# Kernel tuning notes

Measured on AMD Instinct MI355X. Metric: run time of the kernel, lower is better.

## Reference

```python
import jax, jax.numpy as jnp
from jax import lax
import numpy as np

D_MODEL = 768
D_STATE = 16
D_CONV = 4
EXPAND = 2
D_INNER = EXPAND * D_MODEL
BATCH = 2
SEQ = 512


def setup_inputs() -> dict:
    key = jax.random.key(0)
    ks = jax.random.split(key, 8)
    s = 0.02
    return {
        "x": jax.random.normal(ks[0], (BATCH, SEQ, D_MODEL), jnp.float32),
        "W_in": jax.random.normal(ks[1], (2 * D_INNER, D_MODEL), jnp.float32) * s,
        "conv_w": jax.random.normal(ks[2], (D_INNER, 1, D_CONV), jnp.float32) * s,
        "conv_b": jnp.zeros((D_INNER,), jnp.float32),
        "W_x": jax.random.normal(ks[3], (D_INNER + 2 * D_STATE, D_INNER), jnp.float32) * s,
        "W_dt": jax.random.normal(ks[4], (D_INNER, D_INNER), jnp.float32) * s,
        "b_dt": jnp.zeros((D_INNER,), jnp.float32),
        "A_log": jnp.log(jax.random.uniform(ks[5], (D_INNER, D_STATE), jnp.float32, 1e-4, 1.0)),
        "Dp": jnp.ones((D_INNER,), jnp.float32),
        "W_out": jax.random.normal(ks[6], (D_MODEL, D_INNER), jnp.float32) * s,
    }


def parallel_scan_log(log_coeffs, log_values):
    """Faithful port of ParallelScan.parallel_scan_log (Blelchh-style up/down sweep
    in log space). Indices are static, so the Python loop over O(log L) levels is
    trace-time only."""
    B, L, D = log_coeffs.shape
    if L <= 4:
        run = log_values[:, 0]
        outs = [run]
        for i in range(1, L):
            run = jnp.logaddexp(run, log_coeffs[:, i] + log_values[:, i])
            outs.append(run)
        return jnp.stack(outs, axis=1)
    levels = int(np.ceil(np.log2(L)))
    coeffs, values = log_coeffs, log_values
    # up-sweep
    for level in range(levels):
        step = 2 ** (level + 1)
        if step - 1 >= L:
            break
        right = np.arange(step - 1, L, step)
        left = right - 2 ** level
        m = (left >= 0) & (right < L)
        left, right = left[m], right[m]
        if left.size == 0:
            continue
        new_c = coeffs[:, left] + coeffs[:, right]
        new_v = jnp.logaddexp(values[:, left], coeffs[:, right] + values[:, right])
        coeffs = coeffs.at[:, right].set(new_c)
        values = values.at[:, right].set(new_v)
    # down-sweep
    for level in range(levels - 1, -1, -1):
        step = 2 ** (level + 1)
        if step - 1 >= L:
            continue
        right = np.arange(step - 1, L, step)
        left = right - 2 ** level
        m = (left >= 0) & (right < L)
        left, right = left[m], right[m]
        if left.size == 0:
            continue
        tmp = values[:, right]
        new_r = jnp.logaddexp(values[:, left], coeffs[:, right] + values[:, right])
        values = values.at[:, right].set(new_r)
        values = values.at[:, left].set(tmp)
    return values


def reference(x, W_in, conv_w, conv_b, W_x, W_dt, b_dt, A_log, Dp, W_out):
    Bsz, L, _ = x.shape
    xz = x @ W_in.T                                 # [B, L, 2*d_inner]
    x_inner, z = jnp.split(xz, 2, axis=-1)
    # depthwise causal conv1d (pad left d_conv-1, truncate to L == torch slice)
    xc = jnp.transpose(x_inner, (0, 2, 1))          # [B, d_inner, L]
    xc = lax.conv_general_dilated(
        xc, conv_w, (1,), [(D_CONV - 1, 0)],
        dimension_numbers=("NCH", "OIH", "NCH"),
        feature_group_count=D_INNER)
    xc = xc + conv_b[None, :, None]
    x_conv = jax.nn.silu(jnp.transpose(xc, (0, 2, 1)))  # [B, L, d_inner]
    x_dbl = x_conv @ W_x.T                              # [B, L, d_inner + 2*d_state]
    delta, Bmat, Cmat = jnp.split(x_dbl, [D_INNER, D_INNER + D_STATE], axis=-1)
    delta = jax.nn.softplus(delta @ W_dt.T + b_dt)      # [B, L, d_inner]
    # selective scan
    A = -jnp.exp(A_log)                                 # [d_inner, d_state]
    deltaA = jnp.exp(jnp.einsum("bld,dn->bldn", delta, A))
    deltaB_u = jnp.einsum("bld,bln,bld->bldn", delta, Bmat, x_conv)
    log_coeffs = jnp.log(deltaA + 1e-12).reshape(Bsz, L, -1)
    log_values = jnp.log(jnp.abs(deltaB_u) + 1e-12).reshape(Bsz, L, -1)
    scanned = jnp.exp(parallel_scan_log(log_coeffs, log_values))
    scanned = scanned.reshape(Bsz, L, D_INNER, D_STATE)
    y = jnp.einsum("bldn,bln->bld", scanned, Cmat) + x_conv * Dp
    y = y * jax.nn.silu(z)
    return y @ W_out.T
```

## Files before the change

kernel.cpp:

```cpp
#include <hip/hip_runtime.h>
#include <math.h>

#define D_MODEL 768
#define D_STATE 16
#define D_CONV  4
#define D_INNER 1536
#define BATCH   2
#define SEQ     512
#define M_ROWS  (BATCH * SEQ)
#define N_XZ    (2 * D_INNER)
#define N_XDBL  (D_INNER + 2 * D_STATE)

typedef _Float16 half8 __attribute__((ext_vector_type(8)));
typedef float  f32x4  __attribute__((ext_vector_type(4)));
typedef unsigned short ushort_t;
typedef ushort_t ushort8_t __attribute__((ext_vector_type(8)));

__device__ __forceinline__ ushort_t f2h(float f) {
    _Float16 h = (_Float16)f;
    return *(ushort_t*)&h;
}
__device__ __forceinline__ float h2f(ushort_t u) {
    return (float)(*(const _Float16*)&u);
}
__device__ __forceinline__ void pack8(const float* s, ushort_t* d) {
    ushort8_t o;
#pragma unroll
    for (int j = 0; j < 8; ++j) o[j] = f2h(s[j]);
    *(ushort8_t*)d = o;
}
__device__ __forceinline__ void gld16(const ushort_t* g, void* l) {
    __builtin_amdgcn_global_load_lds((const __attribute__((address_space(1))) void*)g,
                                     (__attribute__((address_space(3))) void*)l, 16, 0, 0);
}

#define SX   (M_ROWS * D_MODEL)
#define SW1  (N_XZ * D_MODEL)
#define SW2  (N_XDBL * D_INNER)
#define SWDT (D_INNER * D_INNER)
#define SWO  (D_MODEL * D_INNER)
#define SPACK (SX + SW1 + SW2 + SWDT + SWO)
__global__ __launch_bounds__(256) void pack_kernel(
    const float* __restrict__ x, const float* __restrict__ win,
    const float* __restrict__ wx, const float* __restrict__ wdt,
    const float* __restrict__ wo,
    ushort_t* __restrict__ xs, ushort_t* __restrict__ w1, ushort_t* __restrict__ w2,
    ushort_t* __restrict__ wdt16, ushort_t* __restrict__ wo16)
{
    long i = ((long)blockIdx.x * 256 + threadIdx.x) * 8;
    if (i >= SPACK) return;
    const float* src; ushort_t* dst; long base;
    if (i < SX)                         { src = x;   dst = xs;    base = i; }
    else if (i < SX + SW1)              { src = win; dst = w1;    base = i - SX; }
    else if (i < SX + SW1 + SW2)        { src = wx;  dst = w2;    base = i - SX - SW1; }
    else if (i < SX + SW1 + SW2 + SWDT) { src = wdt; dst = wdt16; base = i - SX - SW1 - SW2; }
    else                                { src = wo;  dst = wo16;  base = i - SX - SW1 - SW2 - SWDT; }
    float v[8];
    *(float4*)(v)     = *(const float4*)(src + base);
    *(float4*)(v + 4) = *(const float4*)(src + base + 4);
    pack8(v, dst + base);
}

template<int HALF_OUT>
__global__ __launch_bounds__(512, 6) void gemm_lds(
    const ushort_t* __restrict__ A, int lda,
    const ushort_t* __restrict__ B, int ldb,
    void* __restrict__ Cbase, long pstride, int ldc,
    int N, int kc)
{
    __shared__ ushort_t smA[3][4096];
    __shared__ ushort_t smB[3][4096];

    const int tid  = threadIdx.x;
    const int w    = tid >> 6;
    const int lane = tid & 63;
    const int lr   = lane & 15;
    const int lq   = lane >> 4;

    const int Gx = gridDim.x, Gy = gridDim.y;
    const int T = Gx * Gy * gridDim.z;
    const int f = blockIdx.x + Gx * (blockIdx.y + Gy * blockIdx.z);
    const int g = (T & 7) ? f : ((f & 7) * (T >> 3) + (f >> 3));
    const int bx = g % Gx;
    const int by = (g / Gx) % Gy;
    const int z  = g / (Gx * Gy);
    ushort_t* __restrict__ Ch = (ushort_t*)Cbase + (long)z * pstride;
    float*    __restrict__ Cf = (float*)Cbase + (long)z * pstride;

    const int bm = by * 128;
    const int bn = bx * 128;
    const int k0base = z * kc;

    auto stage = [&](int buf, int k0) {
        {
            const int rA = bm + w * 16 + lr;
            gld16(A + (long)rA * lda + k0 + lq * 8, &smA[buf][w * 512]);
        }
        {
            int rB = bn + w * 16 + lr; if (rB >= N) rB = N - 1;
            gld16(B + (long)rB * ldb + k0 + lq * 8, &smB[buf][w * 512]);
        }
    };

    f32x4 acc[4][2] = {};
    const int wm = (w & 1) * 64;
    const int wn = (w >> 1) * 32;

    const int nIter = kc >> 5;
    stage(0, k0base);
    int cur = 0;
    for (int it = 0; it < nIter; ++it) {
        const int nxt = (cur == 2) ? 0 : cur + 1;
        if (it + 1 < nIter) {
            stage(nxt, k0base + (it + 1) * 32);
            asm volatile("s_waitcnt vmcnt(2)" ::: "memory");
        } else {
            asm volatile("s_waitcnt vmcnt(0)" ::: "memory");
        }
        __builtin_amdgcn_s_barrier();
        asm volatile("" ::: "memory");

        half8 ah[4], bh[2];
#pragma unroll
        for (int mt = 0; mt < 4; ++mt)
            ah[mt] = *(const half8*)&smA[cur][(((w & 1) * 4 + mt) * 512) + lq * 128 + lr * 8];
#pragma unroll
        for (int nt = 0; nt < 2; ++nt)
            bh[nt] = *(const half8*)&smB[cur][(((w >> 1) * 2 + nt) * 512) + lq * 128 + lr * 8];
#pragma unroll
        for (int mt = 0; mt < 4; ++mt)
#pragma unroll
            for (int nt = 0; nt < 2; ++nt)
                acc[mt][nt] = __builtin_amdgcn_mfma_f32_16x16x32_f16(ah[mt], bh[nt], acc[mt][nt], 0, 0, 0);
        cur = nxt;
    }

#pragma unroll
    for (int mt = 0; mt < 4; ++mt)
#pragma unroll
        for (int nt = 0; nt < 2; ++nt)
#pragma unroll
            for (int r = 0; r < 4; ++r) {
                int row = bm + wm + mt * 16 + lq * 4 + r;
                int col = bn + wn + nt * 16 + lr;
                if (col >= N) continue;
                if (HALF_OUT) Ch[(long)row * ldc + col] = f2h(acc[mt][nt][r]);
                else          Cf[(long)row * ldc + col] = acc[mt][nt][r];
            }
}

__global__ __launch_bounds__(256) void conv_silu_kernel(
    const ushort_t* __restrict__ P, long ps,
    const float* __restrict__ conv_w, const float* __restrict__ conv_b,
    float* __restrict__ xconvT, float* __restrict__ zsiluT,
    ushort_t* __restrict__ xc)
{
    __shared__ float Tx[64][17];
    __shared__ float Tz[64][17];
    const int rb = blockIdx.x;
    const int db = blockIdx.y;
    const int dl = threadIdx.x & 63;
    const int d  = db * 64 + dl;
    const int rr = threadIdx.x >> 6;
    const float w0 = conv_w[d * 4 + 0], w1 = conv_w[d * 4 + 1];
    const float w2 = conv_w[d * 4 + 2], w3 = conv_w[d * 4 + 3];
    const float bb = conv_b[d];
    auto mrg = [&](long o) {
        return h2f(P[o]) + h2f(P[o + ps]) + h2f(P[o + 2 * ps]) + h2f(P[o + 3 * ps]);
    };
#pragma unroll
    for (int q = 0; q < 4; ++q) {
        const int r = rb * 16 + q * 4 + rr;
        const int l = r & (SEQ - 1);
        float acc = bb;
        if (l >= 3) acc = fmaf(w0, mrg((long)(r - 3) * N_XZ + d), acc);
        if (l >= 2) acc = fmaf(w1, mrg((long)(r - 2) * N_XZ + d), acc);
        if (l >= 1) acc = fmaf(w2, mrg((long)(r - 1) * N_XZ + d), acc);
        acc = fmaf(w3, mrg((long)r * N_XZ + d), acc);
        float s = acc / (1.f + expf(-acc));
        xc[(long)r * D_INNER + d] = f2h(s);
        float zv = mrg((long)r * N_XZ + D_INNER + d);
        Tx[dl][q * 4 + rr] = s;
        Tz[dl][q * 4 + rr] = zv / (1.f + expf(-zv));
    }
    __syncthreads();
    const int rp = threadIdx.x & 15;
    const int dp = threadIdx.x >> 4;
#pragma unroll
    for (int p = 0; p < 4; ++p) {
        int dd = p * 16 + dp;
        long o = (long)(db * 64 + dd) * M_ROWS + rb * 16 + rp;
        xconvT[o] = Tx[dd][rp];
        zsiluT[o] = Tz[dd][rp];
    }
}

__global__ __launch_bounds__(256) void ep_xdbl_kernel(
    const float* __restrict__ P, long ps,
    ushort_t* __restrict__ xd, float* __restrict__ BCT)
{
    long i = ((long)blockIdx.x * 256 + threadIdx.x) * 8;
    if (i >= (long)M_ROWS * N_XDBL) return;
    int row = (int)(i / N_XDBL);
    int col = (int)(i - (long)row * N_XDBL);
    float f[8];
#pragma unroll
    for (int j = 0; j < 8; ++j)
        f[j] = P[i + j] + P[i + j + ps] + P[i + j + 2 * ps] + P[i + j + 3 * ps];
    pack8(f, xd + i);
    if (col >= D_INNER) {
#pragma unroll
        for (int j = 0; j < 8; ++j)
            BCT[(long)(col + j - D_INNER) * M_ROWS + row] = f[j];
    }
}

__global__ __launch_bounds__(256) void ep_merge_kernel(
    const ushort_t* __restrict__ P, long ps, float* __restrict__ out)
{
    long i = ((long)blockIdx.x * 256 + threadIdx.x) * 8;
    if (i >= (long)M_ROWS * D_MODEL) return;
    float o[8] = {};
#pragma unroll
    for (int z = 0; z < 16; ++z) {
        ushort8_t v = *(const ushort8_t*)(P + i + z * ps);
#pragma unroll
        for (int j = 0; j < 8; ++j) o[j] += h2f(v[j]);
    }
    *(float4*)(out + i)     = *(float4*)(o);
    *(float4*)(out + i + 4) = *(float4*)(o + 4);
}

__global__ __launch_bounds__(256) void scan_kernel(
    const ushort_t* __restrict__ P, long ps,
    const float* __restrict__ b_dt,
    const float* __restrict__ xconvT,
    const float* __restrict__ zsiluT,
    const float* __restrict__ BCT,
    const float* __restrict__ A_log,
    const float* __restrict__ Dp,
    ushort_t* __restrict__ uT)
{
    __shared__ float dlT[512];
    __shared__ float xrT[512];
    __shared__ float red[3 * 512];

    const int bid = blockIdx.x;
    const int b   = bid / D_INNER;
    const int d   = bid % D_INNER;
    const int tid = threadIdx.x;
    const int w   = tid >> 6;
    const int t   = tid & 63;
    const long od = (long)d * M_ROWS + b * SEQ;

    const float bdt = b_dt[d];
#pragma unroll
    for (int q = 0; q < 2; ++q) {
        const int l = tid + q * 256;
        float v = bdt;
#pragma unroll
        for (int z = 0; z < 8; ++z) v += h2f(P[od + l + z * ps]);
        float sp = fmaxf(v, 0.f) + log1pf(expf(-fabsf(v)));
        const int li = (l & 7) * 64 + (l >> 3);
        dlT[li] = sp;
        xrT[li] = xconvT[od + l];
    }
    __syncthreads();

    float dl[8], xr[8], dx[8], yac[8];
#pragma unroll
    for (int j = 0; j < 8; ++j) {
        dl[j] = dlT[j * 64 + t];
        xr[j] = xrT[j * 64 + t];
        dx[j] = dl[j] * xr[j];
        yac[j] = 0.f;
    }
    const int l0 = 8 * t;

#pragma unroll
    for (int nn = 0; nn < 4; ++nn) {
        const int n = w * 4 + nn;
        const float Adn = -expf(A_log[d * D_STATE + n]);
        const float4* Bp = (const float4*)(BCT + (long)n * M_ROWS + b * SEQ + l0);
        float4 b0 = Bp[0], b1 = Bp[1];
        float Bv[8] = {b0.x, b0.y, b0.z, b0.w, b1.x, b1.y, b1.z, b1.w};
        float c[8], v[8];
#pragma unroll
        for (int j = 0; j < 8; ++j) {
            c[j] = __expf(dl[j] * Adn);
            v[j] = fabsf(dx[j] * Bv[j]);
        }
        float c01 = c[1] * c[0], v01 = fmaf(c[1], v[0], v[1]);
        float c23 = c[3] * c[2], v23 = fmaf(c[3], v[2], v[3]);
        float c45 = c[5] * c[4], v45 = fmaf(c[5], v[4], v[5]);
        float c67 = c[7] * c[6], v67 = fmaf(c[7], v[6], v[7]);
        float c03 = c23 * c01,  v03 = fmaf(c23, v01, v23);
        float c47 = c67 * c45,  v47 = fmaf(c67, v45, v67);
        float cA  = c47 * c03,  vA  = fmaf(c47, v03, v47);
#pragma unroll
        for (int h = 1; h <= 32; h <<= 1) {
            float cl = __shfl_up(cA, (unsigned)h);
            float vl = __shfl_up(vA, (unsigned)h);
            if (t >= h) { vA = fmaf(cA, vl, vA); cA = cA * cl; }
        }
        float s = __shfl_up(vA, 1u);
        if (t == 0) s = 0.f;
        const float4* Cp = (const float4*)(BCT + (long)(16 + n) * M_ROWS + b * SEQ + l0);
        float4 c0 = Cp[0], c1 = Cp[1];
        float Cv[8] = {c0.x, c0.y, c0.z, c0.w, c1.x, c1.y, c1.z, c1.w};
#pragma unroll
        for (int j = 0; j < 8; ++j) {
            s = fmaf(c[j], s, v[j]);
            yac[j] = fmaf(s, Cv[j], yac[j]);
        }
    }

    if (w) {
#pragma unroll
        for (int j = 0; j < 8; ++j) red[(w - 1) * 512 + j * 64 + t] = yac[j];
    }
    __syncthreads();
    if (w == 0) {
        const float Dpd = Dp[d];
        ushort8_t uo;
#pragma unroll
        for (int j = 0; j < 8; ++j) {
            float y = yac[j] + red[j * 64 + t] + red[512 + j * 64 + t] + red[1024 + j * 64 + t];
            float uv = fmaf(xr[j], Dpd, y) * zsiluT[od + l0 + j];
            uo[j] = f2h(uv);
        }
        *(ushort8_t*)(uT + od + l0) = uo;
    }
}

__global__ __launch_bounds__(256) void transpose_split_kernel(
    const ushort_t* __restrict__ uT, ushort_t* __restrict__ u)
{
    __shared__ ushort_t T[64][65];
    const int m0 = blockIdx.x * 64;
    const int d0 = blockIdx.y * 64;
    const int c  = threadIdx.x & 63;
    const int rr = threadIdx.x >> 6;
#pragma unroll
    for (int p = 0; p < 64; p += 4)
        T[p + rr][c] = uT[(long)(d0 + p + rr) * M_ROWS + m0 + c];
    __syncthreads();
#pragma unroll
    for (int p = 0; p < 64; p += 4) {
        int rm = p + rr;
        u[(long)(m0 + rm) * D_INNER + (d0 + c)] = T[c][rm];
    }
}

extern "C" void kernel_launch(void* const* d_in, const int* in_sizes, int n_in,
                              void* d_out, int out_size, void* d_ws, size_t ws_size,
                              hipStream_t stream)
{
    (void)in_sizes; (void)n_in; (void)out_size; (void)ws_size;

    const float* x      = (const float*)d_in[0];
    const float* W_in   = (const float*)d_in[1];
    const float* conv_w = (const float*)d_in[2];
    const float* conv_b = (const float*)d_in[3];
    const float* W_x    = (const float*)d_in[4];
    const float* W_dt   = (const float*)d_in[5];
    const float* b_dt   = (const float*)d_in[6];
    const float* A_log  = (const float*)d_in[7];
    const float* Dp     = (const float*)d_in[8];
    const float* W_out  = (const float*)d_in[9];
    float* out = (float*)d_out;

    float* ws = (float*)d_ws;
    long off = 0;
    float* P      = ws + off; off += 2L * M_ROWS * N_XZ;
    float* uTbuf  = ws + off; off += (long)D_INNER * M_ROWS / 2;
    float* xconvT = ws + off; off += (long)D_INNER * M_ROWS;
    float* zsiluT = ws + off; off += (long)D_INNER * M_ROWS;
    float* xsbuf  = ws + off; off += (long)M_ROWS * D_MODEL / 2;
    float* w1buf  = ws + off; off += (long)N_XZ * D_MODEL / 2;
    float* w2buf  = ws + off; off += (long)N_XDBL * D_INNER / 2;
    float* wdtbuf = ws + off; off += (long)D_INNER * D_INNER / 2;
    float* wobuf  = ws + off; off += (long)D_MODEL * D_INNER / 2;
    float* xcbuf  = ws + off; off += (long)M_ROWS * D_INNER / 2;
    float* xdbuf  = ws + off; off += (long)M_ROWS * N_XDBL / 2;
    float* BCT    = ws + off; off += (long)2 * D_STATE * M_ROWS;

    ushort_t* xs    = (ushort_t*)xsbuf;
    ushort_t* w1    = (ushort_t*)w1buf;
    ushort_t* w2    = (ushort_t*)w2buf;
    ushort_t* wdt16 = (ushort_t*)wdtbuf;
    ushort_t* wo16  = (ushort_t*)wobuf;
    ushort_t* xc    = (ushort_t*)xcbuf;
    ushort_t* xd    = (ushort_t*)xdbuf;
    ushort_t* u_i   = (ushort_t*)xcbuf;
    ushort_t* uT    = (ushort_t*)uTbuf;
    ushort_t* P16   = (ushort_t*)P;

    const long psG1 = (long)M_ROWS * N_XZ;
    const long psG3 = (long)M_ROWS * N_XDBL;
    const long psG4 = (long)D_INNER * M_ROWS;
    const long psG6 = (long)M_ROWS * D_MODEL;

    dim3 blk(256);
    dim3 gblk(512);

    pack_kernel<<<dim3(SPACK / 2048), blk, 0, stream>>>(
        x, W_in, W_x, W_dt, W_out, xs, w1, w2, wdt16, wo16);
    gemm_lds<1><<<dim3(N_XZ / 128, M_ROWS / 128, 4), gblk, 0, stream>>>(
        xs, D_MODEL, w1, D_MODEL, P16, psG1, N_XZ, N_XZ, D_MODEL / 4);
    conv_silu_kernel<<<dim3(M_ROWS / 16, D_INNER / 64), blk, 0, stream>>>(
        P16, psG1, conv_w, conv_b, xconvT, zsiluT, xc);
    gemm_lds<0><<<dim3((N_XDBL + 127) / 128, M_ROWS / 128, 4), gblk, 0, stream>>>(
        xc, D_INNER, w2, D_INNER, P, psG3, N_XDBL, N_XDBL, D_INNER / 4);
    ep_xdbl_kernel<<<dim3((M_ROWS * N_XDBL) / 2048), blk, 0, stream>>>(
        P, psG3, xd, BCT);
    gemm_lds<1><<<dim3(M_ROWS / 128, D_INNER / 128, 8), gblk, 0, stream>>>(
        wdt16, D_INNER, xd, N_XDBL, P16, psG4, M_ROWS, M_ROWS, D_INNER / 8);
    scan_kernel<<<dim3(BATCH * D_INNER), blk, 0, stream>>>(
        P16, psG4, b_dt, xconvT, zsiluT, BCT, A_log, Dp, uT);
    transpose_split_kernel<<<dim3(M_ROWS / 64, D_INNER / 64), blk, 0, stream>>>(
        uT, u_i);
    gemm_lds<1><<<dim3(D_MODEL / 128, M_ROWS / 128, 16), gblk, 0, stream>>>(
        u_i, D_INNER, wo16, D_INNER, P16, psG6, D_MODEL, D_MODEL, D_INNER / 16);
    ep_merge_kernel<<<dim3((M_ROWS * D_MODEL) / 2048), blk, 0, stream>>>(
        P16, psG6, out);
}
```

Before: 206.8 us.

## Fuse all stages into a persistent megakernel with software grid barriers

Replaces the ten separate kernel launches with one persistent kernel of 384 blocks that runs every stage (pack, four GEMMs, conv/silu, epilogues, scan, transpose, merge) in sequence, separated by atomic-counter grid barriers. The goal is to remove launch gaps and tail effects between the many small kernels. Several per-stage parameters change along the way: the W_x GEMM split-K drops from 4 to 3, the conv and transpose tiles are retiled, and the scan handles two channels per block. The cost is that every stage runs on a fixed grid that may not match its natural parallelism, plus barrier spin overhead. The barrier depends on all 384 blocks being co-resident, and its spin loop has a timeout that could silently break synchronization.

```diff
diff --git a/kernel.cpp b/kernel.cpp
--- a/kernel.cpp
+++ b/kernel.cpp
@@ -40,52 +40,58 @@
 #define SWDT (D_INNER * D_INNER)
 #define SWO  (D_MODEL * D_INNER)
 #define SPACK (SX + SW1 + SW2 + SWDT + SWO)
-__global__ __launch_bounds__(256) void pack_kernel(
-    const float* __restrict__ x, const float* __restrict__ win,
-    const float* __restrict__ wx, const float* __restrict__ wdt,
-    const float* __restrict__ wo,
-    ushort_t* __restrict__ xs, ushort_t* __restrict__ w1, ushort_t* __restrict__ w2,
-    ushort_t* __restrict__ wdt16, ushort_t* __restrict__ wo16)
-{
-    long i = ((long)blockIdx.x * 256 + threadIdx.x) * 8;
-    if (i >= SPACK) return;
-    const float* src; ushort_t* dst; long base;
-    if (i < SX)                         { src = x;   dst = xs;    base = i; }
-    else if (i < SX + SW1)              { src = win; dst = w1;    base = i - SX; }
-    else if (i < SX + SW1 + SW2)        { src = wx;  dst = w2;    base = i - SX - SW1; }
-    else if (i < SX + SW1 + SW2 + SWDT) { src = wdt; dst = wdt16; base = i - SX - SW1 - SW2; }
-    else                                { src = wo;  dst = wo16;  base = i - SX - SW1 - SW2 - SWDT; }
-    float v[8];
-    *(float4*)(v)     = *(const float4*)(src + base);
-    *(float4*)(v + 4) = *(const float4*)(src + base + 4);
-    pack8(v, dst + base);
+
+#define PSG1 ((long)M_ROWS * N_XZ)
+#define PSG3 ((long)M_ROWS * N_XDBL)
+#define PSG4 ((long)D_INNER * M_ROWS)
+#define PSG6 ((long)M_ROWS * D_MODEL)
+
+#define NBLK 384
+
+struct Params {
+    const float *x, *W_in, *conv_w, *conv_b, *W_x, *W_dt, *b_dt, *A_log, *Dp, *W_out;
+    float* out;
+    ushort_t *xs, *w1, *w2, *wdt16, *wo16, *xc, *xd, *u_i, *uT, *P16;
+    float *Pf, *xconvT, *zsiluT, *BCT;
+    unsigned* bar;
+};
+
+__device__ __forceinline__ void grid_barrier(unsigned* bar) {
+    __syncthreads();
+    if (threadIdx.x == 0) {
+        __threadfence();
+        unsigned gen = __hip_atomic_load(bar + 1, __ATOMIC_RELAXED, __HIP_MEMORY_SCOPE_AGENT);
+        unsigned prev = __hip_atomic_fetch_add(bar, 1u, __ATOMIC_ACQ_REL, __HIP_MEMORY_SCOPE_AGENT);
+        if (prev == (unsigned)(NBLK - 1)) {
+            __hip_atomic_store(bar, 0u, __ATOMIC_RELAXED, __HIP_MEMORY_SCOPE_AGENT);
+            __hip_atomic_fetch_add(bar + 1, 1u, __ATOMIC_RELEASE, __HIP_MEMORY_SCOPE_AGENT);
+        } else {
+            long spins = 0;
+            while (__hip_atomic_load(bar + 1, __ATOMIC_RELAXED, __HIP_MEMORY_SCOPE_AGENT) == gen) {
+                __builtin_amdgcn_s_sleep(2);
+                if (++spins > (1L << 26)) break;
+            }
+        }
+        __threadfence();
+    }
+    __syncthreads();
 }
 
 template<int HALF_OUT>
-__global__ __launch_bounds__(512, 6) void gemm_lds(
+__device__ __forceinline__ void gemm_tile(
+    ushort_t* smA, ushort_t* smB,
     const ushort_t* __restrict__ A, int lda,
     const ushort_t* __restrict__ B, int ldb,
-    void* __restrict__ Cbase, long pstride, int ldc,
-    int N, int kc)
+    void* Cbase, long pstride, int ldc, int N, int kc,
+    int bx, int by, int z, int tid)
 {
-    __shared__ ushort_t smA[3][4096];
-    __shared__ ushort_t smB[3][4096];
-
-    const int tid  = threadIdx.x;
     const int w    = tid >> 6;
     const int lane = tid & 63;
     const int lr   = lane & 15;
     const int lq   = lane >> 4;
 
-    const int Gx = gridDim.x, Gy = gridDim.y;
-    const int T = Gx * Gy * gridDim.z;
-    const int f = blockIdx.x + Gx * (blockIdx.y + Gy * blockIdx.z);
-    const int g = (T & 7) ? f : ((f & 7) * (T >> 3) + (f >> 3));
-    const int bx = g % Gx;
-    const int by = (g / Gx) % Gy;
-    const int z  = g / (Gx * Gy);
-    ushort_t* __restrict__ Ch = (ushort_t*)Cbase + (long)z * pstride;
-    float*    __restrict__ Cf = (float*)Cbase + (long)z * pstride;
+    ushort_t* Ch = (ushort_t*)Cbase + (long)z * pstride;
+    float*    Cf = (float*)Cbase + (long)z * pstride;
 
     const int bm = by * 128;
     const int bn = bx * 128;
@@ -94,11 +100,11 @@
     auto stage = [&](int buf, int k0) {
         {
             const int rA = bm + w * 16 + lr;
-            gld16(A + (long)rA * lda + k0 + lq * 8, &smA[buf][w * 512]);
+            gld16(A + (long)rA * lda + k0 + lq * 8, smA + buf * 4096 + w * 512);
         }
         {
             int rB = bn + w * 16 + lr; if (rB >= N) rB = N - 1;
-            gld16(B + (long)rB * ldb + k0 + lq * 8, &smB[buf][w * 512]);
+            gld16(B + (long)rB * ldb + k0 + lq * 8, smB + buf * 4096 + w * 512);
         }
     };
 
@@ -123,10 +129,10 @@
         half8 ah[4], bh[2];
 #pragma unroll
         for (int mt = 0; mt < 4; ++mt)
-            ah[mt] = *(const half8*)&smA[cur][(((w & 1) * 4 + mt) * 512) + lq * 128 + lr * 8];
+            ah[mt] = *(const half8*)&smA[cur * 4096 + (((w & 1) * 4 + mt) * 512) + lq * 128 + lr * 8];
 #pragma unroll
         for (int nt = 0; nt < 2; ++nt)
-            bh[nt] = *(const half8*)&smB[cur][(((w >> 1) * 2 + nt) * 512) + lq * 128 + lr * 8];
+            bh[nt] = *(const half8*)&smB[cur * 4096 + (((w >> 1) * 2 + nt) * 512) + lq * 128 + lr * 8];
 #pragma unroll
         for (int mt = 0; mt < 4; ++mt)
 #pragma unroll
@@ -149,206 +155,255 @@
             }
 }
 
-__global__ __launch_bounds__(256) void conv_silu_kernel(
-    const ushort_t* __restrict__ P, long ps,
-    const float* __restrict__ conv_w, const float* __restrict__ conv_b,
-    float* __restrict__ xconvT, float* __restrict__ zsiluT,
-    ushort_t* __restrict__ xc)
+__global__ __launch_bounds__(512, 4) void mega_kernel(Params p)
 {
-    __shared__ float Tx[64][17];
-    __shared__ float Tz[64][17];
-    const int rb = blockIdx.x;
-    const int db = blockIdx.y;
-    const int dl = threadIdx.x & 63;
-    const int d  = db * 64 + dl;
-    const int rr = threadIdx.x >> 6;
-    const float w0 = conv_w[d * 4 + 0], w1 = conv_w[d * 4 + 1];
-    const float w2 = conv_w[d * 4 + 2], w3 = conv_w[d * 4 + 3];
-    const float bb = conv_b[d];
-    auto mrg = [&](long o) {
-        return h2f(P[o]) + h2f(P[o + ps]) + h2f(P[o + 2 * ps]) + h2f(P[o + 3 * ps]);
-    };
-#pragma unroll
-    for (int q = 0; q < 4; ++q) {
-        const int r = rb * 16 + q * 4 + rr;
-        const int l = r & (SEQ - 1);
-        float acc = bb;
-        if (l >= 3) acc = fmaf(w0, mrg((long)(r - 3) * N_XZ + d), acc);
-        if (l >= 2) acc = fmaf(w1, mrg((long)(r - 2) * N_XZ + d), acc);
-        if (l >= 1) acc = fmaf(w2, mrg((long)(r - 1) * N_XZ + d), acc);
-        acc = fmaf(w3, mrg((long)r * N_XZ + d), acc);
-        float s = acc / (1.f + expf(-acc));
-        xc[(long)r * D_INNER + d] = f2h(s);
-        float zv = mrg((long)r * N_XZ + D_INNER + d);
-        Tx[dl][q * 4 + rr] = s;
-        Tz[dl][q * 4 + rr] = zv / (1.f + expf(-zv));
-    }
-    __syncthreads();
-    const int rp = threadIdx.x & 15;
-    const int dp = threadIdx.x >> 4;
-#pragma unroll
-    for (int p = 0; p < 4; ++p) {
-        int dd = p * 16 + dp;
-        long o = (long)(db * 64 + dd) * M_ROWS + rb * 16 + rp;
-        xconvT[o] = Tx[dd][rp];
-        zsiluT[o] = Tz[dd][rp];
-    }
-}
-
-__global__ __launch_bounds__(256) void ep_xdbl_kernel(
-    const float* __restrict__ P, long ps,
-    ushort_t* __restrict__ xd, float* __restrict__ BCT)
-{
-    long i = ((long)blockIdx.x * 256 + threadIdx.x) * 8;
-    if (i >= (long)M_ROWS * N_XDBL) return;
-    int row = (int)(i / N_XDBL);
-    int col = (int)(i - (long)row * N_XDBL);
-    float f[8];
-#pragma unroll
-    for (int j = 0; j < 8; ++j)
-        f[j] = P[i + j] + P[i + j + ps] + P[i + j + 2 * ps] + P[i + j + 3 * ps];
-    pack8(f, xd + i);
-    if (col >= D_INNER) {
+    __shared__ __align__(16) unsigned char smem[49152];
+    ushort_t* smA = (ushort_t*)smem;
+    ushort_t* smB = (ushort_t*)(smem + 24576);
+
+    const int tid = threadIdx.x;
+    const int bid = blockIdx.x;
+    const int NB  = NBLK;
+
+    for (long v = (long)bid * 512 + tid; v < SPACK / 8; v += (long)NB * 512) {
+        long i = v * 8;
+        const float* src; ushort_t* dst; long base;
+        if (i < SX)                         { src = p.x;    dst = p.xs;    base = i; }
+        else if (i < SX + SW1)              { src = p.W_in; dst = p.w1;    base = i - SX; }
+        else if (i < SX + SW1 + SW2)        { src = p.W_x;  dst = p.w2;    base = i - SX - SW1; }
+        else if (i < SX + SW1 + SW2 + SWDT) { src = p.W_dt; dst = p.wdt16; base = i - SX - SW1 - SW2; }
+        else                                { src = p.W_out;dst = p.wo16;  base = i - SX - SW1 - SW2 - SWDT; }
+        float vv[8];
+        *(float4*)(vv)     = *(const float4*)(src + base);
+        *(float4*)(vv + 4) = *(const float4*)(src + base + 4);
+        pack8(vv, dst + base);
+    }
+    grid_barrier(p.bar);
+
+    for (int t = bid; t < 768; t += NB) {
+        gemm_tile<1>(smA, smB, p.xs, D_MODEL, p.w1, D_MODEL,
+                     p.P16, PSG1, N_XZ, N_XZ, D_MODEL / 4,
+                     t % 24, (t / 24) % 8, t / 192, tid);
+        __syncthreads();
+    }
+    grid_barrier(p.bar);
+
+    {
+        float* Tx = (float*)smem;
+        float* Tz = Tx + 64 * 33;
+        const ushort_t* P = p.P16;
+        for (int tu = bid; tu < 768; tu += NB) {
+            const int rb = tu & 31;
+            const int db = tu >> 5;
+            const int dl = tid & 63;
+            const int d  = db * 64 + dl;
+            const int rr = tid >> 6;
+            const float w0 = p.conv_w[d * 4 + 0], w1v = p.conv_w[d * 4 + 1];
+            const float w2v = p.conv_w[d * 4 + 2], w3v = p.conv_w[d * 4 + 3];
+            const float bb = p.conv_b[d];
+            auto mrg = [&](long o) {
+                return h2f(P[o]) + h2f(P[o + PSG1]) + h2f(P[o + 2 * PSG1]) + h2f(P[o + 3 * PSG1]);
+            };
+            __syncthreads();
+#pragma unroll
+            for (int q = 0; q < 4; ++q) {
+                const int r = rb * 32 + q * 8 + rr;
+                const int l = r & (SEQ - 1);
+                float acc = bb;
+                if (l >= 3) acc = fmaf(w0,  mrg((long)(r - 3) * N_XZ + d), acc);
+                if (l >= 2) acc = fmaf(w1v, mrg((long)(r - 2) * N_XZ + d), acc);
+                if (l >= 1) acc = fmaf(w2v, mrg((long)(r - 1) * N_XZ + d), acc);
+                acc = fmaf(w3v, mrg((long)r * N_XZ + d), acc);
+                float s = acc / (1.f + expf(-acc));
+                p.xc[(long)r * D_INNER + d] = f2h(s);
+                float zv = mrg((long)r * N_XZ + D_INNER + d);
+                Tx[dl * 33 + q * 8 + rr] = s;
+                Tz[dl * 33 + q * 8 + rr] = zv / (1.f + expf(-zv));
+            }
+            __syncthreads();
+            const int rp = tid & 31;
+            const int dp = (tid >> 5) & 15;
+#pragma unroll
+            for (int pp = 0; pp < 4; ++pp) {
+                int dd = pp * 16 + dp;
+                long o = (long)(db * 64 + dd) * M_ROWS + rb * 32 + rp;
+                p.xconvT[o] = Tx[dd * 33 + rp];
+                p.zsiluT[o] = Tz[dd * 33 + rp];
+            }
+        }
+    }
+    grid_barrier(p.bar);
+
+    for (int t = bid; t < 312; t += NB) {
+        gemm_tile<0>(smA, smB, p.xc, D_INNER, p.w2, D_INNER,
+                     p.Pf, PSG3, N_XDBL, N_XDBL, D_INNER / 3,
+                     t % 13, (t / 13) % 8, t / 104, tid);
+        __syncthreads();
+    }
+    grid_barrier(p.bar);
+
+    for (long v = (long)bid * 512 + tid; v < (long)M_ROWS * N_XDBL / 8; v += (long)NB * 512) {
+        long i = v * 8;
+        int row = (int)(i / N_XDBL);
+        int col = (int)(i - (long)row * N_XDBL);
+        float f[8];
 #pragma unroll
         for (int j = 0; j < 8; ++j)
-            BCT[(long)(col + j - D_INNER) * M_ROWS + row] = f[j];
-    }
-}
-
-__global__ __launch_bounds__(256) void ep_merge_kernel(
-    const ushort_t* __restrict__ P, long ps, float* __restrict__ out)
-{
-    long i = ((long)blockIdx.x * 256 + threadIdx.x) * 8;
-    if (i >= (long)M_ROWS * D_MODEL) return;
-    float o[8] = {};
-#pragma unroll
-    for (int z = 0; z < 16; ++z) {
-        ushort8_t v = *(const ushort8_t*)(P + i + z * ps);
-#pragma unroll
-        for (int j = 0; j < 8; ++j) o[j] += h2f(v[j]);
-    }
-    *(float4*)(out + i)     = *(float4*)(o);
-    *(float4*)(out + i + 4) = *(float4*)(o + 4);
-}
-
-__global__ __launch_bounds__(256) void scan_kernel(
-    const ushort_t* __restrict__ P, long ps,
-    const float* __restrict__ b_dt,
-    const float* __restrict__ xconvT,
-    const float* __restrict__ zsiluT,
-    const float* __restrict__ BCT,
-    const float* __restrict__ A_log,
-    const float* __restrict__ Dp,
-    ushort_t* __restrict__ uT)
-{
-    __shared__ float dlT[512];
-    __shared__ float xrT[512];
-    __shared__ float red[3 * 512];
-
-    const int bid = blockIdx.x;
-    const int b   = bid / D_INNER;
-    const int d   = bid % D_INNER;
-    const int tid = threadIdx.x;
-    const int w   = tid >> 6;
-    const int t   = tid & 63;
-    const long od = (long)d * M_ROWS + b * SEQ;
-
-    const float bdt = b_dt[d];
-#pragma unroll
-    for (int q = 0; q < 2; ++q) {
-        const int l = tid + q * 256;
-        float v = bdt;
-#pragma unroll
-        for (int z = 0; z < 8; ++z) v += h2f(P[od + l + z * ps]);
-        float sp = fmaxf(v, 0.f) + log1pf(expf(-fabsf(v)));
-        const int li = (l & 7) * 64 + (l >> 3);
-        dlT[li] = sp;
-        xrT[li] = xconvT[od + l];
-    }
-    __syncthreads();
-
-    float dl[8], xr[8], dx[8], yac[8];
-#pragma unroll
-    for (int j = 0; j < 8; ++j) {
-        dl[j] = dlT[j * 64 + t];
-        xr[j] = xrT[j * 64 + t];
-        dx[j] = dl[j] * xr[j];
-        yac[j] = 0.f;
-    }
-    const int l0 = 8 * t;
-
-#pragma unroll
-    for (int nn = 0; nn < 4; ++nn) {
-        const int n = w * 4 + nn;
-        const float Adn = -expf(A_log[d * D_STATE + n]);
-        const float4* Bp = (const float4*)(BCT + (long)n * M_ROWS + b * SEQ + l0);
-        float4 b0 = Bp[0], b1 = Bp[1];
-        float Bv[8] = {b0.x, b0.y, b0.z, b0.w, b1.x, b1.y, b1.z, b1.w};
-        float c[8], v[8];
-#pragma unroll
-        for (int j = 0; j < 8; ++j) {
-            c[j] = __expf(dl[j] * Adn);
-            v[j] = fabsf(dx[j] * Bv[j]);
-        }
-        float c01 = c[1] * c[0], v01 = fmaf(c[1], v[0], v[1]);
-        float c23 = c[3] * c[2], v23 = fmaf(c[3], v[2], v[3]);
-        float c45 = c[5] * c[4], v45 = fmaf(c[5], v[4], v[5]);
-        float c67 = c[7] * c[6], v67 = fmaf(c[7], v[6], v[7]);
-        float c03 = c23 * c01,  v03 = fmaf(c23, v01, v23);
-        float c47 = c67 * c45,  v47 = fmaf(c67, v45, v67);
-        float cA  = c47 * c03,  vA  = fmaf(c47, v03, v47);
-#pragma unroll
-        for (int h = 1; h <= 32; h <<= 1) {
-            float cl = __shfl_up(cA, (unsigned)h);
-            float vl = __shfl_up(vA, (unsigned)h);
-            if (t >= h) { vA = fmaf(cA, vl, vA); cA = cA * cl; }
-        }
-        float s = __shfl_up(vA, 1u);
-        if (t == 0) s = 0.f;
-        const float4* Cp = (const float4*)(BCT + (long)(16 + n) * M_ROWS + b * SEQ + l0);
-        float4 c0 = Cp[0], c1 = Cp[1];
-        float Cv[8] = {c0.x, c0.y, c0.z, c0.w, c1.x, c1.y, c1.z, c1.w};
-#pragma unroll
-        for (int j = 0; j < 8; ++j) {
-            s = fmaf(c[j], s, v[j]);
-            yac[j] = fmaf(s, Cv[j], yac[j]);
-        }
-    }
-
-    if (w) {
-#pragma unroll
-        for (int j = 0; j < 8; ++j) red[(w - 1) * 512 + j * 64 + t] = yac[j];
-    }
-    __syncthreads();
-    if (w == 0) {
-        const float Dpd = Dp[d];
-        ushort8_t uo;
-#pragma unroll
-        for (int j = 0; j < 8; ++j) {
-            float y = yac[j] + red[j * 64 + t] + red[512 + j * 64 + t] + red[1024 + j * 64 + t];
-            float uv = fmaf(xr[j], Dpd, y) * zsiluT[od + l0 + j];
-            uo[j] = f2h(uv);
-        }
-        *(ushort8_t*)(uT + od + l0) = uo;
-    }
-}
-
-__global__ __launch_bounds__(256) void transpose_split_kernel(
-    const ushort_t* __restrict__ uT, ushort_t* __restrict__ u)
-{
-    __shared__ ushort_t T[64][65];
-    const int m0 = blockIdx.x * 64;
-    const int d0 = blockIdx.y * 64;
-    const int c  = threadIdx.x & 63;
-    const int rr = threadIdx.x >> 6;
-#pragma unroll
-    for (int p = 0; p < 64; p += 4)
-        T[p + rr][c] = uT[(long)(d0 + p + rr) * M_ROWS + m0 + c];
-    __syncthreads();
-#pragma unroll
-    for (int p = 0; p < 64; p += 4) {
-        int rm = p + rr;
-        u[(long)(m0 + rm) * D_INNER + (d0 + c)] = T[c][rm];
+            f[j] = p.Pf[i + j] + p.Pf[i + j + PSG3] + p.Pf[i + j + 2 * PSG3];
+        pack8(f, p.xd + i);
+        if (col >= D_INNER) {
+#pragma unroll
+            for (int j = 0; j < 8; ++j)
+                p.BCT[(long)(col + j - D_INNER) * M_ROWS + row] = f[j];
+        }
+    }
+    grid_barrier(p.bar);
+
+    for (int t = bid; t < 768; t += NB) {
+        gemm_tile<1>(smA, smB, p.wdt16, D_INNER, p.xd, N_XDBL,
+                     p.P16, PSG4, M_ROWS, M_ROWS, D_INNER / 8,
+                     t % 8, (t / 8) % 12, t / 96, tid);
+        __syncthreads();
+    }
+    grid_barrier(p.bar);
+
+    {
+        float* S = (float*)smem;
+        const int w    = tid >> 6;
+        const int half = w >> 2;
+        const int wl   = w & 3;
+        const int t64  = tid & 63;
+        float* dlT = S + half * 2560;
+        float* xrT = dlT + 512;
+        float* red = xrT + 512;
+        for (int u = bid; u < 1536; u += NB) {
+            const int bd = 2 * u + half;
+            const int b  = bd / D_INNER;
+            const int d  = bd % D_INNER;
+            const long od = (long)d * M_ROWS + b * SEQ;
+            const float bdt = p.b_dt[d];
+            __syncthreads();
+            const int lh = tid & 255;
+#pragma unroll
+            for (int q = 0; q < 2; ++q) {
+                const int l = lh + q * 256;
+                float v = bdt;
+#pragma unroll
+                for (int z = 0; z < 8; ++z) v += h2f(p.P16[od + l + z * PSG4]);
+                float sp = fmaxf(v, 0.f) + log1pf(expf(-fabsf(v)));
+                const int li = (l & 7) * 64 + (l >> 3);
+                dlT[li] = sp;
+                xrT[li] = p.xconvT[od + l];
+            }
+            __syncthreads();
+
+            float dl[8], xr[8], dx[8], yac[8];
+#pragma unroll
+            for (int j = 0; j < 8; ++j) {
+                dl[j] = dlT[j * 64 + t64];
+                xr[j] = xrT[j * 64 + t64];
+                dx[j] = dl[j] * xr[j];
+                yac[j] = 0.f;
+            }
+            const int l0 = 8 * t64;
+#pragma unroll
+            for (int nn = 0; nn < 4; ++nn) {
+                const int n = wl * 4 + nn;
+                const float Adn = -expf(p.A_log[d * D_STATE + n]);
+                const float4* Bp = (const float4*)(p.BCT + (long)n * M_ROWS + b * SEQ + l0);
+                float4 b0 = Bp[0], b1 = Bp[1];
+                float Bv[8] = {b0.x, b0.y, b0.z, b0.w, b1.x, b1.y, b1.z, b1.w};
+                float c[8], v[8];
+#pragma unroll
+                for (int j = 0; j < 8; ++j) {
+                    c[j] = __expf(dl[j] * Adn);
+                    v[j] = fabsf(dx[j] * Bv[j]);
+                }
+                float c01 = c[1] * c[0], v01 = fmaf(c[1], v[0], v[1]);
+                float c23 = c[3] * c[2], v23 = fmaf(c[3], v[2], v[3]);
+                float c45 = c[5] * c[4], v45 = fmaf(c[5], v[4], v[5]);
+                float c67 = c[7] * c[6], v67 = fmaf(c[7], v[6], v[7]);
+                float c03 = c23 * c01,  v03 = fmaf(c23, v01, v23);
+                float c47 = c67 * c45,  v47 = fmaf(c67, v45, v67);
+                float cA  = c47 * c03,  vA  = fmaf(c47, v03, v47);
+#pragma unroll
+                for (int h = 1; h <= 32; h <<= 1) {
+                    float cl = __shfl_up(cA, (unsigned)h);
+                    float vl = __shfl_up(vA, (unsigned)h);
+                    if (t64 >= h) { vA = fmaf(cA, vl, vA); cA = cA * cl; }
+                }
+                float s = __shfl_up(vA, 1u);
+                if (t64 == 0) s = 0.f;
+                const float4* Cp = (const float4*)(p.BCT + (long)(16 + n) * M_ROWS + b * SEQ + l0);
+                float4 c0 = Cp[0], c1 = Cp[1];
+                float Cv[8] = {c0.x, c0.y, c0.z, c0.w, c1.x, c1.y, c1.z, c1.w};
+#pragma unroll
+                for (int j = 0; j < 8; ++j) {
+                    s = fmaf(c[j], s, v[j]);
+                    yac[j] = fmaf(s, Cv[j], yac[j]);
+                }
+            }
+
+            if (wl) {
+#pragma unroll
+                for (int j = 0; j < 8; ++j) red[(wl - 1) * 512 + j * 64 + t64] = yac[j];
+            }
+            __syncthreads();
+            if (wl == 0) {
+                const float Dpd = p.Dp[d];
+                ushort8_t uo;
+#pragma unroll
+                for (int j = 0; j < 8; ++j) {
+                    float y = yac[j] + red[j * 64 + t64] + red[512 + j * 64 + t64] + red[1024 + j * 64 + t64];
+                    float uv = fmaf(xr[j], Dpd, y) * p.zsiluT[od + l0 + j];
+                    uo[j] = f2h(uv);
+                }
+                *(ushort8_t*)(p.uT + od + l0) = uo;
+            }
+        }
+    }
+    grid_barrier(p.bar);
+
+    {
+        ushort_t* T = (ushort_t*)smem;
+        for (int tu = bid; tu < 384; tu += NB) {
+            const int m0 = (tu & 15) * 64;
+            const int d0 = (tu >> 4) * 64;
+            const int c  = tid & 63;
+            const int rr = tid >> 6;
+            __syncthreads();
+#pragma unroll
+            for (int pp = 0; pp < 64; pp += 8)
+                T[(pp + rr) * 65 + c] = p.uT[(long)(d0 + pp + rr) * M_ROWS + m0 + c];
+            __syncthreads();
+#pragma unroll
+            for (int pp = 0; pp < 64; pp += 8) {
+                int rm = pp + rr;
+                p.u_i[(long)(m0 + rm) * D_INNER + (d0 + c)] = T[c * 65 + rm];
+            }
+        }
+    }
+    grid_barrier(p.bar);
+
+    for (int t = bid; t < 768; t += NB) {
+        gemm_tile<1>(smA, smB, p.u_i, D_INNER, p.wo16, D_INNER,
+                     p.P16, PSG6, D_MODEL, D_MODEL, D_INNER / 16,
+                     t % 6, (t / 6) % 8, t / 48, tid);
+        __syncthreads();
+    }
+    grid_barrier(p.bar);
+
+    for (long v = (long)bid * 512 + tid; v < (long)M_ROWS * D_MODEL / 8; v += (long)NB * 512) {
+        long i = v * 8;
+        float o[8] = {};
+#pragma unroll
+        for (int z = 0; z < 16; ++z) {
+            ushort8_t vv = *(const ushort8_t*)(p.P16 + i + z * PSG6);
+#pragma unroll
+            for (int j = 0; j < 8; ++j) o[j] += h2f(vv[j]);
+        }
+        *(float4*)(p.out + i)     = *(float4*)(o);
+        *(float4*)(p.out + i + 4) = *(float4*)(o + 4);
     }
 }
 
@@ -358,24 +413,25 @@
 {
     (void)in_sizes; (void)n_in; (void)out_size; (void)ws_size;
 
-    const float* x      = (const float*)d_in[0];
-    const float* W_in   = (const float*)d_in[1];
-    const float* conv_w = (const float*)d_in[2];
-    const float* conv_b = (const float*)d_in[3];
-    const float* W_x    = (const float*)d_in[4];
-    const float* W_dt   = (const float*)d_in[5];
-    const float* b_dt   = (const float*)d_in[6];
-    const float* A_log  = (const float*)d_in[7];
-    const float* Dp     = (const float*)d_in[8];
-    const float* W_out  = (const float*)d_in[9];
-    float* out = (float*)d_out;
+    Params p;
+    p.x      = (const float*)d_in[0];
+    p.W_in   = (const float*)d_in[1];
+    p.conv_w = (const float*)d_in[2];
+    p.conv_b = (const float*)d_in[3];
+    p.W_x    = (const float*)d_in[4];
+    p.W_dt   = (const float*)d_in[5];
+    p.b_dt   = (const float*)d_in[6];
+    p.A_log  = (const float*)d_in[7];
+    p.Dp     = (const float*)d_in[8];
+    p.W_out  = (const float*)d_in[9];
+    p.out    = (float*)d_out;
 
     float* ws = (float*)d_ws;
     long off = 0;
     float* P      = ws + off; off += 2L * M_ROWS * N_XZ;
-    float* uTbuf  = ws + off; off += (long)D_INNER * M_ROWS / 2;
     float* xconvT = ws + off; off += (long)D_INNER * M_ROWS;
     float* zsiluT = ws + off; off += (long)D_INNER * M_ROWS;
+    float* uTbuf  = ws + off; off += (long)D_INNER * M_ROWS / 2;
     float* xsbuf  = ws + off; off += (long)M_ROWS * D_MODEL / 2;
     float* w1buf  = ws + off; off += (long)N_XZ * D_MODEL / 2;
     float* w2buf  = ws + off; off += (long)N_XDBL * D_INNER / 2;
@@ -384,44 +440,25 @@
     float* xcbuf  = ws + off; off += (long)M_ROWS * D_INNER / 2;
     float* xdbuf  = ws + off; off += (long)M_ROWS * N_XDBL / 2;
     float* BCT    = ws + off; off += (long)2 * D_STATE * M_ROWS;
-
-    ushort_t* xs    = (ushort_t*)xsbuf;
-    ushort_t* w1    = (ushort_t*)w1buf;
-    ushort_t* w2    = (ushort_t*)w2buf;
-    ushort_t* wdt16 = (ushort_t*)wdtbuf;
-    ushort_t* wo16  = (ushort_t*)wobuf;
-    ushort_t* xc    = (ushort_t*)xcbuf;
-    ushort_t* xd    = (ushort_t*)xdbuf;
-    ushort_t* u_i   = (ushort_t*)xcbuf;
-    ushort_t* uT    = (ushort_t*)uTbuf;
-    ushort_t* P16   = (ushort_t*)P;
-
-    const long psG1 = (long)M_ROWS * N_XZ;
-    const long psG3 = (long)M_ROWS * N_XDBL;
-    const long psG4 = (long)D_INNER * M_ROWS;
-    const long psG6 = (long)M_ROWS * D_MODEL;
-
-    dim3 blk(256);
-    dim3 gblk(512);
-
-    pack_kernel<<<dim3(SPACK / 2048), blk, 0, stream>>>(
-        x, W_in, W_x, W_dt, W_out, xs, w1, w2, wdt16, wo16);
-    gemm_lds<1><<<dim3(N_XZ / 128, M_ROWS / 128, 4), gblk, 0, stream>>>(
-        xs, D_MODEL, w1, D_MODEL, P16, psG1, N_XZ, N_XZ, D_MODEL / 4);
-    conv_silu_kernel<<<dim3(M_ROWS / 16, D_INNER / 64), blk, 0, stream>>>(
-        P16, psG1, conv_w, conv_b, xconvT, zsiluT, xc);
-    gemm_lds<0><<<dim3((N_XDBL + 127) / 128, M_ROWS / 128, 4), gblk, 0, stream>>>(
-        xc, D_INNER, w2, D_INNER, P, psG3, N_XDBL, N_XDBL, D_INNER / 4);
-    ep_xdbl_kernel<<<dim3((M_ROWS * N_XDBL) / 2048), blk, 0, stream>>>(
-        P, psG3, xd, BCT);
-    gemm_lds<1><<<dim3(M_ROWS / 128, D_INNER / 128, 8), gblk, 0, stream>>>(
-        wdt16, D_INNER, xd, N_XDBL, P16, psG4, M_ROWS, M_ROWS, D_INNER / 8);
-    scan_kernel<<<dim3(BATCH * D_INNER), blk, 0, stream>>>(
-        P16, psG4, b_dt, xconvT, zsiluT, BCT, A_log, Dp, uT);
-    transpose_split_kernel<<<dim3(M_ROWS / 64, D_INNER / 64), blk, 0, stream>>>(
-        uT, u_i);
-    gemm_lds<1><<<dim3(D_MODEL / 128, M_ROWS / 128, 16), gblk, 0, stream>>>(
-        u_i, D_INNER, wo16, D_INNER, P16, psG6, D_MODEL, D_MODEL, D_INNER / 16);
-    ep_merge_kernel<<<dim3((M_ROWS * D_MODEL) / 2048), blk, 0, stream>>>(
-        P16, psG6, out);
-}
+    off = (off + 63) & ~63L;
+    unsigned* bar = (unsigned*)(ws + off);
+
+    p.xs    = (ushort_t*)xsbuf;
+    p.w1    = (ushort_t*)w1buf;
+    p.w2    = (ushort_t*)w2buf;
+    p.wdt16 = (ushort_t*)wdtbuf;
+    p.wo16  = (ushort_t*)wobuf;
+    p.xc    = (ushort_t*)xcbuf;
+    p.xd    = (ushort_t*)xdbuf;
+    p.u_i   = (ushort_t*)xcbuf;
+    p.uT    = (ushort_t*)uTbuf;
+    p.P16   = (ushort_t*)P;
+    p.Pf    = P;
+    p.xconvT = xconvT;
+    p.zsiluT = zsiluT;
+    p.BCT    = BCT;
+    p.bar    = bar;
+
+    hipMemsetAsync(bar, 0, 64, stream);
+    mega_kernel<<<dim3(NBLK), dim3(512), 0, stream>>>(p);
+}
```

Result: slower. 772.8 us (+273.7%).
